# Kernel optimization log

Measured on AMD Instinct MI355X. Metric: run time of the kernel, lower is better.

Reference implementation:

```python
import jax, jax.numpy as jnp
import numpy as np

N_NODES = 100000
N_EDGES = 600000
DIM = 128
LN_EPS = 1e-5


def setup_inputs() -> dict:
    key = jax.random.key(0)
    ks = jax.random.split(key, 12)
    s = 1.0 / np.sqrt(DIM)
    return {
        "h": jax.random.normal(ks[0], (N_NODES, DIM), dtype=jnp.float32),
        "edge_src": jax.random.randint(ks[1], (N_EDGES,), 0, N_NODES, dtype=jnp.int32),
        "edge_dst": jax.random.randint(ks[2], (N_EDGES,), 0, N_NODES, dtype=jnp.int32),
        "W_self": jax.random.uniform(ks[3], (DIM, DIM), jnp.float32, -s, s),
        "b_self": jax.random.uniform(ks[4], (DIM,), jnp.float32, -s, s),
        "W_neigh": jax.random.uniform(ks[5], (DIM, DIM), jnp.float32, -s, s),
        "b_neigh": jax.random.uniform(ks[6], (DIM,), jnp.float32, -s, s),
        "W_gate": jax.random.uniform(ks[7], (DIM, 2 * DIM), jnp.float32, -s, s),
        "b_gate": jax.random.uniform(ks[8], (DIM,), jnp.float32, -s, s),
        "ln_gamma": jnp.ones((DIM,), jnp.float32),
        "ln_beta": jnp.zeros((DIM,), jnp.float32),
    }


def reference(h, edge_src, edge_dst, W_self, b_self, W_neigh, b_neigh, W_gate, b_gate, ln_gamma, ln_beta):
    n = h.shape[0]
    # self transform: [N, D]
    hs = h @ W_self.T + b_self
    # mean over predecessors via segment sum over edges (src -> dst)
    neigh_sum = jax.ops.segment_sum(h[edge_src], edge_dst, num_segments=n)
    counts = jax.ops.segment_sum(jnp.ones((edge_src.shape[0],), h.dtype), edge_dst, num_segments=n)
    has_pred = (counts > 0).astype(h.dtype)[:, None]
    neigh_mean = neigh_sum / jnp.maximum(counts, 1.0)[:, None]
    hn = neigh_mean @ W_neigh.T + b_neigh
    # nodes with no predecessors skip the neighbor term entirely (incl. bias)
    m = hs + has_pred * hn
    gate = jax.nn.sigmoid(jnp.concatenate([h, m], axis=-1) @ W_gate.T + b_gate)
    v = gate * m + (1.0 - gate) * h
    # LayerNorm (biased variance, as torch) + relu
    mu = jnp.mean(v, axis=-1, keepdims=True)
    var = jnp.mean(jnp.square(v - mu), axis=-1, keepdims=True)
    out = (v - mu) * jax.lax.rsqrt(var + LN_EPS) * ln_gamma + ln_beta
    return jax.nn.relu(out)
```

## Files before the change

### kernel.cpp

```cpp
#include <hip/hip_runtime.h>
#include <math.h>

#define N_NODES 100000
#define N_EDGES 600000
#define DIM 128
#define LN_EPS 1e-5f
#define SCAN_NBLK ((N_NODES + 255) / 256)
#define NTILES ((N_NODES + 127) / 128)
#define NODE_GRID 256

typedef __bf16 bf16x8 __attribute__((ext_vector_type(8)));
typedef __bf16 bf16x4 __attribute__((ext_vector_type(4)));
typedef float f32x4 __attribute__((ext_vector_type(4)));

__global__ __launch_bounds__(256)
void prep_kernel(const float* __restrict__ h, const int* __restrict__ edst,
                 __bf16* __restrict__ h_bf, int* __restrict__ counts) {
  int i = blockIdx.x * 256 + threadIdx.x;
  {
    const float4 v0 = *reinterpret_cast<const float4*>(h + (size_t)i * 8);
    const float4 v1 = *reinterpret_cast<const float4*>(h + (size_t)i * 8 + 4);
    bf16x8 b;
    b[0] = (__bf16)v0.x; b[1] = (__bf16)v0.y; b[2] = (__bf16)v0.z; b[3] = (__bf16)v0.w;
    b[4] = (__bf16)v1.x; b[5] = (__bf16)v1.y; b[6] = (__bf16)v1.z; b[7] = (__bf16)v1.w;
    *reinterpret_cast<bf16x8*>(h_bf + (size_t)i * 8) = b;
  }
  if (i < N_EDGES) atomicAdd(&counts[edst[i]], 1);
}

__global__ __launch_bounds__(256)
void scan1_kernel(const int* __restrict__ counts, int* __restrict__ block_sums) {
  int i = blockIdx.x * 256 + threadIdx.x;
  int v = (i < N_NODES) ? counts[i] : 0;
#pragma unroll
  for (int off = 1; off < 64; off <<= 1) v += __shfl_xor(v, off);
  __shared__ int ws[4];
  if ((threadIdx.x & 63) == 0) ws[threadIdx.x >> 6] = v;
  __syncthreads();
  if (threadIdx.x == 0) block_sums[blockIdx.x] = ws[0] + ws[1] + ws[2] + ws[3];
}

__global__ __launch_bounds__(512)
void scan2_kernel(int* __restrict__ block_sums) {
  __shared__ int sh[512];
  int t = threadIdx.x;
  int v = (t < SCAN_NBLK) ? block_sums[t] : 0;
  sh[t] = v;
  __syncthreads();
#pragma unroll
  for (int off = 1; off < 512; off <<= 1) {
    int u = (t >= off) ? sh[t - off] : 0;
    __syncthreads();
    sh[t] += u;
    __syncthreads();
  }
  if (t < SCAN_NBLK) block_sums[t] = (t == 0) ? 0 : sh[t - 1];
}

__global__ __launch_bounds__(256)
void scan3_kernel(const int* __restrict__ counts, const int* __restrict__ block_excl,
                  int* __restrict__ row_off, int* __restrict__ cursor) {
  int i = blockIdx.x * 256 + threadIdx.x;
  int t = threadIdx.x;
  int lane = t & 63, wv = t >> 6;
  int v = (i < N_NODES) ? counts[i] : 0;
  int s = v;
#pragma unroll
  for (int off = 1; off < 64; off <<= 1) {
    int u = __shfl_up(s, off);
    if (lane >= off) s += u;
  }
  __shared__ int wtot[4];
  if (lane == 63) wtot[wv] = s;
  __syncthreads();
  int wo = 0;
  for (int w = 0; w < wv; ++w) wo += wtot[w];
  int excl = block_excl[blockIdx.x] + wo + (s - v);
  if (i < N_NODES) { row_off[i] = excl; cursor[i] = 0; }
  if (i == 0) row_off[N_NODES] = N_EDGES;
}

__global__ void csr_fill_kernel(const int* __restrict__ esrc, const int* __restrict__ edst,
                                const int* __restrict__ row_off, int* __restrict__ cursor,
                                int* __restrict__ csr_src) {
  int e = blockIdx.x * 256 + threadIdx.x;
  if (e >= N_EDGES) return;
  int d = edst[e];
  int pos = atomicAdd(&cursor[d], 1);
  csr_src[row_off[d] + pos] = esrc[e];
}

__global__ __launch_bounds__(256)
void gather_kernel(const __bf16* __restrict__ h_bf, const int* __restrict__ csr_src,
                   const int* __restrict__ row_off, __bf16* __restrict__ mean_bf) {
  int node = blockIdx.x * 8 + (threadIdx.x >> 5);
  if (node >= N_NODES) return;
  int t = threadIdx.x & 31;
  int b = row_off[node], e = row_off[node + 1];
  float acc0 = 0.f, acc1 = 0.f, acc2 = 0.f, acc3 = 0.f;
  int i = b;
  for (; i + 4 <= e; i += 4) {
    int s0 = csr_src[i], s1 = csr_src[i + 1], s2 = csr_src[i + 2], s3 = csr_src[i + 3];
    bf16x4 v0 = *reinterpret_cast<const bf16x4*>(h_bf + (size_t)s0 * DIM + t * 4);
    bf16x4 v1 = *reinterpret_cast<const bf16x4*>(h_bf + (size_t)s1 * DIM + t * 4);
    bf16x4 v2 = *reinterpret_cast<const bf16x4*>(h_bf + (size_t)s2 * DIM + t * 4);
    bf16x4 v3 = *reinterpret_cast<const bf16x4*>(h_bf + (size_t)s3 * DIM + t * 4);
    acc0 += (float)v0[0] + (float)v1[0] + (float)v2[0] + (float)v3[0];
    acc1 += (float)v0[1] + (float)v1[1] + (float)v2[1] + (float)v3[1];
    acc2 += (float)v0[2] + (float)v1[2] + (float)v2[2] + (float)v3[2];
    acc3 += (float)v0[3] + (float)v1[3] + (float)v2[3] + (float)v3[3];
  }
  for (; i < e; ++i) {
    int s = csr_src[i];
    bf16x4 v = *reinterpret_cast<const bf16x4*>(h_bf + (size_t)s * DIM + t * 4);
    acc0 += (float)v[0]; acc1 += (float)v[1]; acc2 += (float)v[2]; acc3 += (float)v[3];
  }
  float inv = (e > b) ? 1.0f / (float)(e - b) : 0.0f;
  bf16x4 mv;
  mv[0] = (__bf16)(acc0 * inv); mv[1] = (__bf16)(acc1 * inv);
  mv[2] = (__bf16)(acc2 * inv); mv[3] = (__bf16)(acc3 * inv);
  *reinterpret_cast<bf16x4*>(mean_bf + (size_t)node * DIM + t * 4) = mv;
}

__global__ __launch_bounds__(512, 1)
void node_kernel(const __bf16* __restrict__ h_bf,
                 const __bf16* __restrict__ mean_bf,
                 const int* __restrict__ counts,
                 const float* __restrict__ Wself,
                 const float* __restrict__ Wneigh,
                 const float* __restrict__ Wgate,
                 const float* __restrict__ b_self,
                 const float* __restrict__ b_neigh,
                 const float* __restrict__ b_gate,
                 const float* __restrict__ ln_g,
                 const float* __restrict__ ln_b,
                 float* __restrict__ out) {
  __shared__ __align__(16) char smem[163840];
  char* Wl = smem;

  const int tid = threadIdx.x;

  for (int c = tid; c < 8192; c += 512) {
    int mi = c >> 11;
    int w = c & 2047;
    int row = w >> 4, col8 = w & 15;
    const float* src;
    if (mi == 0)      src = Wself  + row * 128 + col8 * 8;
    else if (mi == 1) src = Wneigh + row * 128 + col8 * 8;
    else if (mi == 2) src = Wgate  + row * 256 + col8 * 8;
    else              src = Wgate  + row * 256 + 128 + col8 * 8;
    float4 v0 = *reinterpret_cast<const float4*>(src);
    float4 v1 = *reinterpret_cast<const float4*>(src + 4);
    bf16x8 b;
    b[0] = (__bf16)v0.x; b[1] = (__bf16)v0.y; b[2] = (__bf16)v0.z; b[3] = (__bf16)v0.w;
    b[4] = (__bf16)v1.x; b[5] = (__bf16)v1.y; b[6] = (__bf16)v1.z; b[7] = (__bf16)v1.w;
    int byte = (row * 256 + col8 * 16) ^ ((row & 7) << 4);
    *reinterpret_cast<bf16x8*>(Wl + mi * 32768 + byte) = b;
  }
  __syncthreads();

  const int lane = tid & 63;
  const int wave = tid >> 6;
  const int col = lane & 15;
  const int kb = (lane >> 4) << 3;
  const int rloc = (lane >> 4) << 2;
  char* Ms = smem + 131072 + wave * 4096;

  for (int tile = blockIdx.x; tile < NTILES; tile += NODE_GRID) {
    const int node0 = tile * 128;

    bf16x8 a_h[4], a_m[4];
    {
      int n_a = node0 + wave * 16 + col;
      if (n_a < N_NODES) {
#pragma unroll
        for (int k0 = 0; k0 < 4; ++k0) {
          int koff = k0 * 32 + kb;
          a_h[k0] = *reinterpret_cast<const bf16x8*>(h_bf + (size_t)n_a * DIM + koff);
          a_m[k0] = *reinterpret_cast<const bf16x8*>(mean_bf + (size_t)n_a * DIM + koff);
        }
      } else {
#pragma unroll
        for (int k0 = 0; k0 < 4; ++k0)
#pragma unroll
          for (int j = 0; j < 8; ++j) { a_h[k0][j] = (__bf16)0.f; a_m[k0][j] = (__bf16)0.f; }
      }
    }

    int4 c4 = *reinterpret_cast<const int4*>(counts + node0 + wave * 16 + rloc);
    float hp[4];
    {
      int nb0 = node0 + wave * 16 + rloc;
      hp[0] = (nb0 + 0 < N_NODES && c4.x > 0) ? 1.f : 0.f;
      hp[1] = (nb0 + 1 < N_NODES && c4.y > 0) ? 1.f : 0.f;
      hp[2] = (nb0 + 2 < N_NODES && c4.z > 0) ? 1.f : 0.f;
      hp[3] = (nb0 + 3 < N_NODES && c4.w > 0) ? 1.f : 0.f;
    }

    f32x4 sacc[8], nacc[8];
#pragma unroll
    for (int i = 0; i < 8; ++i) {
      sacc[i] = (f32x4){0.f, 0.f, 0.f, 0.f};
      nacc[i] = (f32x4){0.f, 0.f, 0.f, 0.f};
    }
#pragma unroll
    for (int k0 = 0; k0 < 4; ++k0) {
      int koff2 = (k0 * 32 + kb) * 2;
#pragma unroll
      for (int nb = 0; nb < 8; ++nb) {
        int row = nb * 16 + col;
        int swz = (row * 256 + koff2) ^ ((row & 7) << 4);
        bf16x8 bs = *reinterpret_cast<const bf16x8*>(Wl + swz);
        bf16x8 bn = *reinterpret_cast<const bf16x8*>(Wl + 32768 + swz);
        sacc[nb] = __builtin_amdgcn_mfma_f32_16x16x32_bf16(a_h[k0], bs, sacc[nb], 0, 0, 0);
        nacc[nb] = __builtin_amdgcn_mfma_f32_16x16x32_bf16(a_m[k0], bn, nacc[nb], 0, 0, 0);
      }
    }

#pragma unroll
    for (int nb = 0; nb < 8; ++nb) {
      int d = nb * 16 + col;
      float bs = b_self[d], bn = b_neigh[d];
#pragma unroll
      for (int r = 0; r < 4; ++r) {
        float mval = sacc[nb][r] + bs + hp[r] * (nacc[nb][r] + bn);
        sacc[nb][r] = mval;
        int rl = rloc + r;
        int byte = (rl * 256 + d * 2) ^ ((rl & 7) << 4);
        *reinterpret_cast<__bf16*>(Ms + byte) = (__bf16)mval;
      }
    }

    f32x4 gacc[8];
#pragma unroll
    for (int i = 0; i < 8; ++i) gacc[i] = (f32x4){0.f, 0.f, 0.f, 0.f};
#pragma unroll
    for (int k0 = 0; k0 < 4; ++k0) {
      int koff2 = (k0 * 32 + kb) * 2;
      int abyte = (col * 256 + koff2) ^ ((col & 7) << 4);
      bf16x8 am2 = *reinterpret_cast<const bf16x8*>(Ms + abyte);
#pragma unroll
      for (int nb = 0; nb < 8; ++nb) {
        int row = nb * 16 + col;
        int swz = (row * 256 + koff2) ^ ((row & 7) << 4);
        bf16x8 bgh = *reinterpret_cast<const bf16x8*>(Wl + 65536 + swz);
        bf16x8 bgm = *reinterpret_cast<const bf16x8*>(Wl + 98304 + swz);
        gacc[nb] = __builtin_amdgcn_mfma_f32_16x16x32_bf16(a_h[k0], bgh, gacc[nb], 0, 0, 0);
        gacc[nb] = __builtin_amdgcn_mfma_f32_16x16x32_bf16(am2, bgm, gacc[nb], 0, 0, 0);
      }
    }

#pragma unroll
    for (int k0 = 0; k0 < 4; ++k0) {
      int byte = (col * 256 + (k0 * 32 + kb) * 2) ^ ((col & 7) << 4);
      *reinterpret_cast<bf16x8*>(Ms + byte) = a_h[k0];
    }

    float s1[4] = {0.f, 0.f, 0.f, 0.f}, s2[4] = {0.f, 0.f, 0.f, 0.f};
#pragma unroll
    for (int nb = 0; nb < 8; ++nb) {
      int d = nb * 16 + col;
      float bg = b_gate[d];
#pragma unroll
      for (int r = 0; r < 4; ++r) {
        int rl = rloc + r;
        int byte = (rl * 256 + d * 2) ^ ((rl & 7) << 4);
        float hval = (float)*reinterpret_cast<const __bf16*>(Ms + byte);
        float g = 1.0f / (1.0f + __expf(-(gacc[nb][r] + bg)));
        float v = g * sacc[nb][r] + (1.0f - g) * hval;
        s1[r] += v;
        s2[r] += v * v;
        *reinterpret_cast<__bf16*>(Ms + byte) = (__bf16)v;
      }
    }
#pragma unroll
    for (int off = 1; off < 16; off <<= 1) {
#pragma unroll
      for (int r = 0; r < 4; ++r) {
        s1[r] += __shfl_xor(s1[r], off);
        s2[r] += __shfl_xor(s2[r], off);
      }
    }
    float mu[4], rs[4];
#pragma unroll
    for (int r = 0; r < 4; ++r) {
      mu[r] = s1[r] * (1.0f / DIM);
      float var = s2[r] * (1.0f / DIM) - mu[r] * mu[r];
      rs[r] = rsqrtf(var + LN_EPS);
    }

    {
      int orow = lane >> 2;
      int ochunk = lane & 3;
      int gn = node0 + wave * 16 + orow;
      int rsel = orow & 3;
      float muv = (rsel & 2) ? ((rsel & 1) ? mu[3] : mu[2]) : ((rsel & 1) ? mu[1] : mu[0]);
      float rsv = (rsel & 2) ? ((rsel & 1) ? rs[3] : rs[2]) : ((rsel & 1) ? rs[1] : rs[0]);
      bool valid = gn < N_NODES;
#pragma unroll
      for (int j = 0; j < 4; ++j) {
        int d0 = ochunk * 8 + j * 32;
        int byte = (orow * 256 + d0 * 2) ^ ((orow & 7) << 4);
        bf16x8 vb = *reinterpret_cast<const bf16x8*>(Ms + byte);
        float4 g0 = *reinterpret_cast<const float4*>(ln_g + d0);
        float4 g1 = *reinterpret_cast<const float4*>(ln_g + d0 + 4);
        float4 e0 = *reinterpret_cast<const float4*>(ln_b + d0);
        float4 e1 = *reinterpret_cast<const float4*>(ln_b + d0 + 4);
        float4 o0, o1;
        o0.x = fmaxf(((float)vb[0] - muv) * rsv * g0.x + e0.x, 0.f);
        o0.y = fmaxf(((float)vb[1] - muv) * rsv * g0.y + e0.y, 0.f);
        o0.z = fmaxf(((float)vb[2] - muv) * rsv * g0.z + e0.z, 0.f);
        o0.w = fmaxf(((float)vb[3] - muv) * rsv * g0.w + e0.w, 0.f);
        o1.x = fmaxf(((float)vb[4] - muv) * rsv * g1.x + e1.x, 0.f);
        o1.y = fmaxf(((float)vb[5] - muv) * rsv * g1.y + e1.y, 0.f);
        o1.z = fmaxf(((float)vb[6] - muv) * rsv * g1.z + e1.z, 0.f);
        o1.w = fmaxf(((float)vb[7] - muv) * rsv * g1.w + e1.w, 0.f);
        if (valid) {
          *reinterpret_cast<float4*>(out + (size_t)gn * DIM + d0) = o0;
          *reinterpret_cast<float4*>(out + (size_t)gn * DIM + d0 + 4) = o1;
        }
      }
    }
  }
}

extern "C" void kernel_launch(void* const* d_in, const int* in_sizes, int n_in,
                              void* d_out, int out_size, void* d_ws, size_t ws_size,
                              hipStream_t stream) {
  const float* h      = (const float*)d_in[0];
  const int*   esrc   = (const int*)d_in[1];
  const int*   edst   = (const int*)d_in[2];
  const float* Wself  = (const float*)d_in[3];
  const float* bself  = (const float*)d_in[4];
  const float* Wneigh = (const float*)d_in[5];
  const float* bneigh = (const float*)d_in[6];
  const float* Wgate  = (const float*)d_in[7];
  const float* bgate  = (const float*)d_in[8];
  const float* ln_g   = (const float*)d_in[9];
  const float* ln_b   = (const float*)d_in[10];
  float* out = (float*)d_out;

  char* ws = (char*)d_ws;
  int* counts   = (int*)ws;
  int* row_off  = (int*)(ws + 400384);
  int* cursor   = (int*)(ws + 800768);
  int* csr_src  = (int*)(ws + 1200768);
  int* blk_sums = (int*)(ws + 3600768);
  __bf16* h_bf    = (__bf16*)(ws + 3602432);
  __bf16* mean_bf = (__bf16*)(ws + 29202432);

  hipMemsetAsync(counts, 0, (size_t)N_NODES * sizeof(int), stream);

  prep_kernel<<<6250, 256, 0, stream>>>(h, edst, h_bf, counts);
  scan1_kernel<<<SCAN_NBLK, 256, 0, stream>>>(counts, blk_sums);
  scan2_kernel<<<1, 512, 0, stream>>>(blk_sums);
  scan3_kernel<<<SCAN_NBLK, 256, 0, stream>>>(counts, blk_sums, row_off, cursor);
  csr_fill_kernel<<<(N_EDGES + 255) / 256, 256, 0, stream>>>(esrc, edst, row_off, cursor, csr_src);
  gather_kernel<<<(N_NODES + 7) / 8, 256, 0, stream>>>(h_bf, csr_src, row_off, mean_bf);
  node_kernel<<<NODE_GRID, 512, 0, stream>>>(
      h_bf, mean_bf, counts, Wself, Wneigh, Wgate,
      bself, bneigh, bgate, ln_g, ln_b, out);
}
```

Before: 157.5 us.

## Vectorize CSR fill and gather, prefetch next tile, reshape gate/LayerNorm epilogue

The CSR fill now processes four edges per thread using int4 loads. The gather uses 16 threads per node with 8-wide bf16 loads. The node kernel prefetches the next tile's h and mean fragments into registers while the current tile is being computed. The gate epilogue is restructured: gate logits go through shared memory into A-fragment layout, so the LayerNorm reduction needs only two cross-lane shuffles and h comes from registers instead of shared memory. This raises register pressure in node_kernel. Storing gate logits and m in bf16 adds some rounding.

```diff
diff --git a/kernel.cpp b/kernel.cpp
--- a/kernel.cpp
+++ b/kernel.cpp
@@ -80,46 +80,64 @@
   if (i == 0) row_off[N_NODES] = N_EDGES;
 }
 
-__global__ void csr_fill_kernel(const int* __restrict__ esrc, const int* __restrict__ edst,
-                                const int* __restrict__ row_off, int* __restrict__ cursor,
-                                int* __restrict__ csr_src) {
-  int e = blockIdx.x * 256 + threadIdx.x;
-  if (e >= N_EDGES) return;
-  int d = edst[e];
-  int pos = atomicAdd(&cursor[d], 1);
-  csr_src[row_off[d] + pos] = esrc[e];
+__global__ __launch_bounds__(256)
+void csr_fill_kernel(const int* __restrict__ esrc, const int* __restrict__ edst,
+                     const int* __restrict__ row_off, int* __restrict__ cursor,
+                     int* __restrict__ csr_src) {
+  int base = (blockIdx.x * 256 + threadIdx.x) * 4;
+  if (base >= N_EDGES) return;
+  int4 s4 = *reinterpret_cast<const int4*>(esrc + base);
+  int4 d4 = *reinterpret_cast<const int4*>(edst + base);
+  {
+    int pos = atomicAdd(&cursor[d4.x], 1);
+    csr_src[row_off[d4.x] + pos] = s4.x;
+  }
+  {
+    int pos = atomicAdd(&cursor[d4.y], 1);
+    csr_src[row_off[d4.y] + pos] = s4.y;
+  }
+  {
+    int pos = atomicAdd(&cursor[d4.z], 1);
+    csr_src[row_off[d4.z] + pos] = s4.z;
+  }
+  {
+    int pos = atomicAdd(&cursor[d4.w], 1);
+    csr_src[row_off[d4.w] + pos] = s4.w;
+  }
 }
 
 __global__ __launch_bounds__(256)
 void gather_kernel(const __bf16* __restrict__ h_bf, const int* __restrict__ csr_src,
                    const int* __restrict__ row_off, __bf16* __restrict__ mean_bf) {
-  int node = blockIdx.x * 8 + (threadIdx.x >> 5);
+  int node = blockIdx.x * 16 + (threadIdx.x >> 4);
   if (node >= N_NODES) return;
-  int t = threadIdx.x & 31;
+  int t = threadIdx.x & 15;
   int b = row_off[node], e = row_off[node + 1];
-  float acc0 = 0.f, acc1 = 0.f, acc2 = 0.f, acc3 = 0.f;
+  float acc[8];
+#pragma unroll
+  for (int j = 0; j < 8; ++j) acc[j] = 0.f;
   int i = b;
   for (; i + 4 <= e; i += 4) {
     int s0 = csr_src[i], s1 = csr_src[i + 1], s2 = csr_src[i + 2], s3 = csr_src[i + 3];
-    bf16x4 v0 = *reinterpret_cast<const bf16x4*>(h_bf + (size_t)s0 * DIM + t * 4);
-    bf16x4 v1 = *reinterpret_cast<const bf16x4*>(h_bf + (size_t)s1 * DIM + t * 4);
-    bf16x4 v2 = *reinterpret_cast<const bf16x4*>(h_bf + (size_t)s2 * DIM + t * 4);
-    bf16x4 v3 = *reinterpret_cast<const bf16x4*>(h_bf + (size_t)s3 * DIM + t * 4);
-    acc0 += (float)v0[0] + (float)v1[0] + (float)v2[0] + (float)v3[0];
-    acc1 += (float)v0[1] + (float)v1[1] + (float)v2[1] + (float)v3[1];
-    acc2 += (float)v0[2] + (float)v1[2] + (float)v2[2] + (float)v3[2];
-    acc3 += (float)v0[3] + (float)v1[3] + (float)v2[3] + (float)v3[3];
+    bf16x8 v0 = *reinterpret_cast<const bf16x8*>(h_bf + (size_t)s0 * DIM + t * 8);
+    bf16x8 v1 = *reinterpret_cast<const bf16x8*>(h_bf + (size_t)s1 * DIM + t * 8);
+    bf16x8 v2 = *reinterpret_cast<const bf16x8*>(h_bf + (size_t)s2 * DIM + t * 8);
+    bf16x8 v3 = *reinterpret_cast<const bf16x8*>(h_bf + (size_t)s3 * DIM + t * 8);
+#pragma unroll
+    for (int j = 0; j < 8; ++j)
+      acc[j] += (float)v0[j] + (float)v1[j] + (float)v2[j] + (float)v3[j];
   }
   for (; i < e; ++i) {
     int s = csr_src[i];
-    bf16x4 v = *reinterpret_cast<const bf16x4*>(h_bf + (size_t)s * DIM + t * 4);
-    acc0 += (float)v[0]; acc1 += (float)v[1]; acc2 += (float)v[2]; acc3 += (float)v[3];
+    bf16x8 v = *reinterpret_cast<const bf16x8*>(h_bf + (size_t)s * DIM + t * 8);
+#pragma unroll
+    for (int j = 0; j < 8; ++j) acc[j] += (float)v[j];
   }
   float inv = (e > b) ? 1.0f / (float)(e - b) : 0.0f;
-  bf16x4 mv;
-  mv[0] = (__bf16)(acc0 * inv); mv[1] = (__bf16)(acc1 * inv);
-  mv[2] = (__bf16)(acc2 * inv); mv[3] = (__bf16)(acc3 * inv);
-  *reinterpret_cast<bf16x4*>(mean_bf + (size_t)node * DIM + t * 4) = mv;
+  bf16x8 mv;
+#pragma unroll
+  for (int j = 0; j < 8; ++j) mv[j] = (__bf16)(acc[j] * inv);
+  *reinterpret_cast<bf16x8*>(mean_bf + (size_t)node * DIM + t * 8) = mv;
 }
 
 __global__ __launch_bounds__(512, 1)
@@ -166,26 +184,29 @@
   const int rloc = (lane >> 4) << 2;
   char* Ms = smem + 131072 + wave * 4096;
 
+  auto load_frags = [&](int tile, bf16x8* fh, bf16x8* fm) {
+    int n_a = tile * 128 + wave * 16 + col;
+    if (n_a < N_NODES) {
+#pragma unroll
+      for (int k0 = 0; k0 < 4; ++k0) {
+        int koff = k0 * 32 + kb;
+        fh[k0] = *reinterpret_cast<const bf16x8*>(h_bf + (size_t)n_a * DIM + koff);
+        fm[k0] = *reinterpret_cast<const bf16x8*>(mean_bf + (size_t)n_a * DIM + koff);
+      }
+    } else {
+#pragma unroll
+      for (int k0 = 0; k0 < 4; ++k0)
+#pragma unroll
+        for (int j = 0; j < 8; ++j) { fh[k0][j] = (__bf16)0.f; fm[k0][j] = (__bf16)0.f; }
+    }
+  };
+
+  bf16x8 a_h[4], a_m[4];
+  load_frags(blockIdx.x, a_h, a_m);
+
   for (int tile = blockIdx.x; tile < NTILES; tile += NODE_GRID) {
     const int node0 = tile * 128;
-
-    bf16x8 a_h[4], a_m[4];
-    {
-      int n_a = node0 + wave * 16 + col;
-      if (n_a < N_NODES) {
-#pragma unroll
-        for (int k0 = 0; k0 < 4; ++k0) {
-          int koff = k0 * 32 + kb;
-          a_h[k0] = *reinterpret_cast<const bf16x8*>(h_bf + (size_t)n_a * DIM + koff);
-          a_m[k0] = *reinterpret_cast<const bf16x8*>(mean_bf + (size_t)n_a * DIM + koff);
-        }
-      } else {
-#pragma unroll
-        for (int k0 = 0; k0 < 4; ++k0)
-#pragma unroll
-          for (int j = 0; j < 8; ++j) { a_h[k0][j] = (__bf16)0.f; a_m[k0][j] = (__bf16)0.f; }
-      }
-    }
+    const int next = tile + NODE_GRID;
 
     int4 c4 = *reinterpret_cast<const int4*>(counts + node0 + wave * 16 + rloc);
     float hp[4];
@@ -224,13 +245,15 @@
 #pragma unroll
       for (int r = 0; r < 4; ++r) {
         float mval = sacc[nb][r] + bs + hp[r] * (nacc[nb][r] + bn);
-        sacc[nb][r] = mval;
         int rl = rloc + r;
         int byte = (rl * 256 + d * 2) ^ ((rl & 7) << 4);
         *reinterpret_cast<__bf16*>(Ms + byte) = (__bf16)mval;
       }
     }
-
+    bf16x8 p_h[4], p_m[4];
+    if (next < NTILES) load_frags(next, p_h, p_m);
+
+    bf16x8 am2[4];
     f32x4 gacc[8];
 #pragma unroll
     for (int i = 0; i < 8; ++i) gacc[i] = (f32x4){0.f, 0.f, 0.f, 0.f};
@@ -238,7 +261,7 @@
     for (int k0 = 0; k0 < 4; ++k0) {
       int koff2 = (k0 * 32 + kb) * 2;
       int abyte = (col * 256 + koff2) ^ ((col & 7) << 4);
-      bf16x8 am2 = *reinterpret_cast<const bf16x8*>(Ms + abyte);
+      am2[k0] = *reinterpret_cast<const bf16x8*>(Ms + abyte);
 #pragma unroll
       for (int nb = 0; nb < 8; ++nb) {
         int row = nb * 16 + col;
@@ -246,80 +269,79 @@
         bf16x8 bgh = *reinterpret_cast<const bf16x8*>(Wl + 65536 + swz);
         bf16x8 bgm = *reinterpret_cast<const bf16x8*>(Wl + 98304 + swz);
         gacc[nb] = __builtin_amdgcn_mfma_f32_16x16x32_bf16(a_h[k0], bgh, gacc[nb], 0, 0, 0);
-        gacc[nb] = __builtin_amdgcn_mfma_f32_16x16x32_bf16(am2, bgm, gacc[nb], 0, 0, 0);
-      }
-    }
-
-#pragma unroll
-    for (int k0 = 0; k0 < 4; ++k0) {
-      int byte = (col * 256 + (k0 * 32 + kb) * 2) ^ ((col & 7) << 4);
-      *reinterpret_cast<bf16x8*>(Ms + byte) = a_h[k0];
-    }
-
-    float s1[4] = {0.f, 0.f, 0.f, 0.f}, s2[4] = {0.f, 0.f, 0.f, 0.f};
+        gacc[nb] = __builtin_amdgcn_mfma_f32_16x16x32_bf16(am2[k0], bgm, gacc[nb], 0, 0, 0);
+      }
+    }
+
 #pragma unroll
     for (int nb = 0; nb < 8; ++nb) {
       int d = nb * 16 + col;
-      float bg = b_gate[d];
 #pragma unroll
       for (int r = 0; r < 4; ++r) {
         int rl = rloc + r;
         int byte = (rl * 256 + d * 2) ^ ((rl & 7) << 4);
-        float hval = (float)*reinterpret_cast<const __bf16*>(Ms + byte);
-        float g = 1.0f / (1.0f + __expf(-(gacc[nb][r] + bg)));
-        float v = g * sacc[nb][r] + (1.0f - g) * hval;
-        s1[r] += v;
-        s2[r] += v * v;
-        *reinterpret_cast<__bf16*>(Ms + byte) = (__bf16)v;
-      }
-    }
-#pragma unroll
-    for (int off = 1; off < 16; off <<= 1) {
-#pragma unroll
-      for (int r = 0; r < 4; ++r) {
-        s1[r] += __shfl_xor(s1[r], off);
-        s2[r] += __shfl_xor(s2[r], off);
-      }
-    }
-    float mu[4], rs[4];
-#pragma unroll
-    for (int r = 0; r < 4; ++r) {
-      mu[r] = s1[r] * (1.0f / DIM);
-      float var = s2[r] * (1.0f / DIM) - mu[r] * mu[r];
-      rs[r] = rsqrtf(var + LN_EPS);
-    }
+        *reinterpret_cast<__bf16*>(Ms + byte) = (__bf16)gacc[nb][r];
+      }
+    }
+    bf16x8 gt[4];
+#pragma unroll
+    for (int k0 = 0; k0 < 4; ++k0) {
+      int abyte = (col * 256 + (k0 * 32 + kb) * 2) ^ ((col & 7) << 4);
+      gt[k0] = *reinterpret_cast<const bf16x8*>(Ms + abyte);
+    }
+
+    float s1 = 0.f, s2 = 0.f;
+    bf16x8 vb[4];
+#pragma unroll
+    for (int k0 = 0; k0 < 4; ++k0) {
+      int c0 = k0 * 32 + kb;
+      float4 bg0 = *reinterpret_cast<const float4*>(b_gate + c0);
+      float4 bg1 = *reinterpret_cast<const float4*>(b_gate + c0 + 4);
+      float bgv[8] = {bg0.x, bg0.y, bg0.z, bg0.w, bg1.x, bg1.y, bg1.z, bg1.w};
+#pragma unroll
+      for (int j = 0; j < 8; ++j) {
+        float g = 1.0f / (1.0f + __expf(-((float)gt[k0][j] + bgv[j])));
+        float v = g * (float)am2[k0][j] + (1.0f - g) * (float)a_h[k0][j];
+        s1 += v;
+        s2 += v * v;
+        vb[k0][j] = (__bf16)v;
+      }
+    }
+    s1 += __shfl_xor(s1, 16); s1 += __shfl_xor(s1, 32);
+    s2 += __shfl_xor(s2, 16); s2 += __shfl_xor(s2, 32);
+    float mu = s1 * (1.0f / DIM);
+    float var = s2 * (1.0f / DIM) - mu * mu;
+    float rs = rsqrtf(var + LN_EPS);
 
     {
-      int orow = lane >> 2;
-      int ochunk = lane & 3;
-      int gn = node0 + wave * 16 + orow;
-      int rsel = orow & 3;
-      float muv = (rsel & 2) ? ((rsel & 1) ? mu[3] : mu[2]) : ((rsel & 1) ? mu[1] : mu[0]);
-      float rsv = (rsel & 2) ? ((rsel & 1) ? rs[3] : rs[2]) : ((rsel & 1) ? rs[1] : rs[0]);
+      int gn = node0 + wave * 16 + col;
       bool valid = gn < N_NODES;
 #pragma unroll
-      for (int j = 0; j < 4; ++j) {
-        int d0 = ochunk * 8 + j * 32;
-        int byte = (orow * 256 + d0 * 2) ^ ((orow & 7) << 4);
-        bf16x8 vb = *reinterpret_cast<const bf16x8*>(Ms + byte);
-        float4 g0 = *reinterpret_cast<const float4*>(ln_g + d0);
-        float4 g1 = *reinterpret_cast<const float4*>(ln_g + d0 + 4);
-        float4 e0 = *reinterpret_cast<const float4*>(ln_b + d0);
-        float4 e1 = *reinterpret_cast<const float4*>(ln_b + d0 + 4);
+      for (int k0 = 0; k0 < 4; ++k0) {
+        int c0 = k0 * 32 + kb;
+        float4 g0 = *reinterpret_cast<const float4*>(ln_g + c0);
+        float4 g1 = *reinterpret_cast<const float4*>(ln_g + c0 + 4);
+        float4 e0 = *reinterpret_cast<const float4*>(ln_b + c0);
+        float4 e1 = *reinterpret_cast<const float4*>(ln_b + c0 + 4);
         float4 o0, o1;
-        o0.x = fmaxf(((float)vb[0] - muv) * rsv * g0.x + e0.x, 0.f);
-        o0.y = fmaxf(((float)vb[1] - muv) * rsv * g0.y + e0.y, 0.f);
-        o0.z = fmaxf(((float)vb[2] - muv) * rsv * g0.z + e0.z, 0.f);
-        o0.w = fmaxf(((float)vb[3] - muv) * rsv * g0.w + e0.w, 0.f);
-        o1.x = fmaxf(((float)vb[4] - muv) * rsv * g1.x + e1.x, 0.f);
-        o1.y = fmaxf(((float)vb[5] - muv) * rsv * g1.y + e1.y, 0.f);
-        o1.z = fmaxf(((float)vb[6] - muv) * rsv * g1.z + e1.z, 0.f);
-        o1.w = fmaxf(((float)vb[7] - muv) * rsv * g1.w + e1.w, 0.f);
+        o0.x = fmaxf(((float)vb[k0][0] - mu) * rs * g0.x + e0.x, 0.f);
+        o0.y = fmaxf(((float)vb[k0][1] - mu) * rs * g0.y + e0.y, 0.f);
+        o0.z = fmaxf(((float)vb[k0][2] - mu) * rs * g0.z + e0.z, 0.f);
+        o0.w = fmaxf(((float)vb[k0][3] - mu) * rs * g0.w + e0.w, 0.f);
+        o1.x = fmaxf(((float)vb[k0][4] - mu) * rs * g1.x + e1.x, 0.f);
+        o1.y = fmaxf(((float)vb[k0][5] - mu) * rs * g1.y + e1.y, 0.f);
+        o1.z = fmaxf(((float)vb[k0][6] - mu) * rs * g1.z + e1.z, 0.f);
+        o1.w = fmaxf(((float)vb[k0][7] - mu) * rs * g1.w + e1.w, 0.f);
         if (valid) {
-          *reinterpret_cast<float4*>(out + (size_t)gn * DIM + d0) = o0;
-          *reinterpret_cast<float4*>(out + (size_t)gn * DIM + d0 + 4) = o1;
+          *reinterpret_cast<float4*>(out + (size_t)gn * DIM + c0) = o0;
+          *reinterpret_cast<float4*>(out + (size_t)gn * DIM + c0 + 4) = o1;
         }
       }
+    }
+
+    if (next < NTILES) {
+#pragma unroll
+      for (int k0 = 0; k0 < 4; ++k0) { a_h[k0] = p_h[k0]; a_m[k0] = p_m[k0]; }
     }
   }
 }
@@ -355,8 +377,8 @@
   scan1_kernel<<<SCAN_NBLK, 256, 0, stream>>>(counts, blk_sums);
   scan2_kernel<<<1, 512, 0, stream>>>(blk_sums);
   scan3_kernel<<<SCAN_NBLK, 256, 0, stream>>>(counts, blk_sums, row_off, cursor);
-  csr_fill_kernel<<<(N_EDGES + 255) / 256, 256, 0, stream>>>(esrc, edst, row_off, cursor, csr_src);
-  gather_kernel<<<(N_NODES + 7) / 8, 256, 0, stream>>>(h_bf, csr_src, row_off, mean_bf);
+  csr_fill_kernel<<<(N_EDGES / 4 + 255) / 256, 256, 0, stream>>>(esrc, edst, row_off, cursor, csr_src);
+  gather_kernel<<<(N_NODES + 15) / 16, 256, 0, stream>>>(h_bf, csr_src, row_off, mean_bf);
   node_kernel<<<NODE_GRID, 512, 0, stream>>>(
       h_bf, mean_bf, counts, Wself, Wneigh, Wgate,
       bself, bneigh, bgate, ln_g, ln_b, out);
```

Result: slower. 172.5 us (+9.5%).
